# Performance work log

Hardware: AMD Instinct MI355X
Metric: run time of the kernel (lower is better)

## Reference

```python
import jax, jax.numpy as jnp
import numpy as np

EMBED_DIM = 256
NUM_HEADS = 4
HEAD_DIM = EMBED_DIM // NUM_HEADS
B, N0, N1 = 4, 2048, 2048


def setup_inputs() -> dict:
    key = jax.random.key(0)
    ks = jax.random.split(key, 16)
    d = EMBED_DIM
    s = 0.02
    return {
        "x0": jax.random.normal(ks[0], (B, N0, d), jnp.float32),
        "x1": jax.random.normal(ks[1], (B, N1, d), jnp.float32),
        "Wqk": jax.random.normal(ks[2], (d, d), jnp.float32) * s,
        "bqk": jnp.zeros((d,), jnp.float32),
        "Wv": jax.random.normal(ks[3], (d, d), jnp.float32) * s,
        "bv": jnp.zeros((d,), jnp.float32),
        "Wout": jax.random.normal(ks[4], (d, d), jnp.float32) * s,
        "bout": jnp.zeros((d,), jnp.float32),
        "W0": jax.random.normal(ks[5], (2 * d, 2 * d), jnp.float32) * s,
        "b0": jnp.zeros((2 * d,), jnp.float32),
        "ln_scale": jnp.ones((2 * d,), jnp.float32),
        "ln_bias": jnp.zeros((2 * d,), jnp.float32),
        "W3": jax.random.normal(ks[6], (2 * d, d), jnp.float32) * s,
        "b3": jnp.zeros((d,), jnp.float32),
    }


def _heads(t, b, n):
    # [b, n, d] -> [b, h, n, hd]
    return t.reshape(b, n, NUM_HEADS, HEAD_DIM).transpose(0, 2, 1, 3)


def _layernorm(y, scale, bias, eps=1e-5):
    mu = jnp.mean(y, axis=-1, keepdims=True)
    var = jnp.mean(jnp.square(y - mu), axis=-1, keepdims=True)
    return (y - mu) * jax.lax.rsqrt(var + eps) * scale + bias


def reference(x0, x1, Wqk, bqk, Wv, bv, Wout, bout, W0, b0, ln_scale, ln_bias, W3, b3):
    b, n0, d = x0.shape
    _, n1, _ = x1.shape
    scale = 1.0 / jnp.sqrt(jnp.float32(HEAD_DIM))

    qk0 = _heads(x0 @ Wqk + bqk, b, n0)
    qk1 = _heads(x1 @ Wqk + bqk, b, n1)
    v0 = _heads(x0 @ Wv + bv, b, n0)
    v1 = _heads(x1 @ Wv + bv, b, n1)

    # shared logits: [b, h, n0, n1]
    logits01 = jnp.einsum('bhid,bhjd->bhij', qk0, qk1) * scale
    attn01 = jax.nn.softmax(logits01, axis=-1)
    m0 = jnp.einsum('bhij,bhjd->bhid', attn01, v1)
    attn10 = jax.nn.softmax(logits01.transpose(0, 1, 3, 2), axis=-1)
    m1 = jnp.einsum('bhji,bhjd->bhid', attn10.transpose(0, 1, 3, 2), v0)

    m0 = m0.transpose(0, 2, 1, 3).reshape(b, n0, d) @ Wout + bout
    m1 = m1.transpose(0, 2, 1, 3).reshape(b, n1, d) @ Wout + bout

    def ffn(x, m):
        y = jnp.concatenate([x, m], axis=-1) @ W0 + b0
        y = _layernorm(y, ln_scale, ln_bias)
        y = jax.nn.gelu(y, approximate=False)
        return x + y @ W3 + b3

    return ffn(x0, m0), ffn(x1, m1)
```

## Files before the change

### kernel.cpp

```cpp
#include <hip/hip_runtime.h>
#include <math.h>

#define BATCH 4
#define SEQ 2048
#define DMODEL 256
#define NH 4
#define HD 64
#define MROWS 8192
#define QKSCALE 0.4246608905f

typedef short bf16x8 __attribute__((ext_vector_type(8)));
typedef float f32x4 __attribute__((ext_vector_type(4)));
typedef unsigned short us;

#if __has_builtin(__builtin_amdgcn_exp2f)
#define EXP2(x) __builtin_amdgcn_exp2f(x)
#else
#define EXP2(x) exp2f(x)
#endif

__device__ __forceinline__ us f2bf(float x) {
  union { float f; unsigned int u; } v;
  v.f = x;
  unsigned int r = (v.u + 0x7FFF + ((v.u >> 16) & 1)) >> 16;
  return (us)r;
}
__device__ __forceinline__ float bf2f(us u) {
  union { unsigned int u; float f; } v;
  v.u = ((unsigned int)u) << 16;
  return v.f;
}
__device__ __forceinline__ unsigned int fbits(float x) {
  union { float f; unsigned int u; } v;
  v.f = x;
  return v.u;
}
__device__ __forceinline__ unsigned int pk2bf(float lo, float hi) {
  return __builtin_amdgcn_perm(fbits(hi), fbits(lo), 0x07060302u);
}
__device__ __forceinline__ void dma16(const void* g, void* l) {
  auto gp = (const __attribute__((address_space(1))) unsigned int*)(unsigned long long)(uintptr_t)g;
  auto lp = (__attribute__((address_space(3))) unsigned int*)(unsigned int)(uintptr_t)l;
  __builtin_amdgcn_global_load_lds(gp, lp, 16, 0, 0);
}

__global__ __launch_bounds__(256) void prep_k(
    const float* __restrict__ x0, const float* __restrict__ x1,
    const float* __restrict__ Wqk, const float* __restrict__ Wv,
    const float* __restrict__ W0, const float* __restrict__ W3,
    const float* __restrict__ Wout,
    const float* __restrict__ bqk, const float* __restrict__ bv,
    const float* __restrict__ b0, const float* __restrict__ bout,
    us* __restrict__ x0b, us* __restrict__ x1b,
    us* __restrict__ Wqvt, us* __restrict__ W1t, us* __restrict__ W3t,
    float* __restrict__ bias_qv, float* __restrict__ bias1) {
  const int bid = blockIdx.x, t = threadIdx.x;
  if (bid < 4096) {
    const int n4 = (MROWS * DMODEL) / 4;
    int i = bid * 256 + t;
    const float* src = (i < n4) ? x0 : x1;
    us* dst = (i < n4) ? x0b : x1b;
    int j = (i < n4) ? i : i - n4;
    float4 v = *(const float4*)&src[j * 4];
    ushort4 o = {f2bf(v.x), f2bf(v.y), f2bf(v.z), f2bf(v.w)};
    *(ushort4*)&dst[j * 4] = o;
  } else if (bid < 5634) {
    int gid = (bid - 4096) * 256 + t;
    if (gid < 65536) {
      int k = gid >> 8, j = gid & 255;
      Wqvt[j * 256 + k] = f2bf(Wqk[gid]);
    } else if (gid < 131072) {
      int i = gid - 65536;
      int k = i >> 8, j = i & 255;
      Wqvt[(256 + j) * 256 + k] = f2bf(Wv[i]);
    } else if (gid < 262144) {
      int i = gid - 131072;
      int k = i >> 9, j = i & 511;
      W1t[j * 512 + k] = f2bf(W0[i]);
    } else if (gid < 393216) {
      int i = gid - 262144;
      int k = i >> 8, j = i & 255;
      W3t[j * 512 + k] = f2bf(W3[i]);
    } else if (gid < 393728) {
      int j = gid - 393216;
      bias_qv[j] = (j < 256) ? bqk[j] : bv[j - 256];
    }
  } else {
    int i = bid - 5634;
    if (i < 256) {
      float a0 = 0.f, a1 = 0.f;
      for (int k0 = 0; k0 < 256; k0 += 8) {
        float wk[8], r0[8], r1[8];
#pragma unroll
        for (int u = 0; u < 8; ++u) {
          wk[u] = Wout[i * 256 + k0 + u];
          const float* row = &W0[(size_t)(256 + k0 + u) * 512];
          r0[u] = row[t];
          r1[u] = row[t + 256];
        }
#pragma unroll
        for (int u = 0; u < 8; ++u) { a0 += wk[u] * r0[u]; a1 += wk[u] * r1[u]; }
      }
      W1t[t * 512 + 256 + i] = f2bf(a0);
      W1t[(t + 256) * 512 + 256 + i] = f2bf(a1);
    } else {
      float a0 = b0[t], a1 = b0[t + 256];
      for (int k = 0; k < 256; ++k) {
        float bk = bout[k];
        const float* row = &W0[(size_t)(256 + k) * 512];
        a0 += bk * row[t];
        a1 += bk * row[t + 256];
      }
      bias1[t] = a0;
      bias1[t + 256] = a1;
    }
  }
}

template <int MODE>
__global__ __launch_bounds__(256) void gemm5(
    const us* __restrict__ A0, const us* __restrict__ A1,
    const us* __restrict__ Am0, const us* __restrict__ Am1,
    const us* __restrict__ Wt, const float* __restrict__ bias,
    const float* __restrict__ r0_, const float* __restrict__ r1_,
    void* __restrict__ C0_, void* __restrict__ C1_,
    void* __restrict__ V0_, void* __restrict__ V1_, int K) {
  constexpr int CT = (MODE == 2) ? 64 : 128;
  constexpr int BG = (CT / 16) * 2;
  constexpr int BUFS = 8192 + BG * 512;
  __shared__ us lds[2 * BUFS];

  const int t = threadIdx.x, w = t >> 6, lane = t & 63;
  const int qd = lane >> 4, l15 = lane & 15;

  const int flat = blockIdx.x + 64 * (blockIdx.y + 4 * blockIdx.z);
  const int xcd = flat & 7, slot = flat >> 3;
  const int xz = (xcd << 4) + (slot >> 2);
  const int bx = xz & 63, z = xz >> 6, coltile = slot & 3;
  const int row0 = bx * 128, col0 = coltile * CT;

  const us* Ax = z ? A1 : A0;
  const us* Am = z ? Am1 : Am0;
  const int qr = (MODE == 2) ? w : (w >> 1);
  const int qc = (MODE == 2) ? 0 : (w & 1);
  constexpr int MI = (MODE == 2) ? 2 : 4;

  f32x4 acc[MI][4];
#pragma unroll
  for (int i = 0; i < MI; ++i)
#pragma unroll
    for (int j = 0; j < 4; ++j) acc[i][j] = (f32x4){0.f, 0.f, 0.f, 0.f};

  const int NK = K >> 6;
#pragma unroll
  for (int pp = 0; pp < (16 + BG) / 4; ++pp) {
    int g = pp * 4 + w;
    const us* src;
    if (g < 16) {
      int tm = g >> 1, s = g & 1;
      int kk = s * 32 + qd * 8;
      src = &((MODE == 1) ? Ax : Ax)[(size_t)(row0 + tm * 16 + l15) * ((MODE == 1) ? 256 : K) + kk];
    } else {
      int gb = g - 16, tn = gb >> 1, s = gb & 1;
      src = &Wt[(size_t)(col0 + tn * 16 + l15) * K + s * 32 + qd * 8];
    }
    dma16(src, &lds[g * 512]);
  }
  __syncthreads();

  int bsel = 0;
  for (int it = 0; it < NK; ++it) {
    if (it + 1 < NK) {
      int k0 = (it + 1) << 6;
#pragma unroll
      for (int pp = 0; pp < (16 + BG) / 4; ++pp) {
        int g = pp * 4 + w;
        const us* src;
        if (g < 16) {
          int tm = g >> 1, s = g & 1;
          const us* Ap = Ax;
          int kk = k0 + s * 32 + qd * 8, lda = K;
          if (MODE == 1) {
            Ap = (k0 < 256) ? Ax : Am;
            kk &= 255;
            lda = 256;
          }
          src = &Ap[(size_t)(row0 + tm * 16 + l15) * lda + kk];
        } else {
          int gb = g - 16, tn = gb >> 1, s = gb & 1;
          src = &Wt[(size_t)(col0 + tn * 16 + l15) * K + k0 + s * 32 + qd * 8];
        }
        dma16(src, &lds[(bsel ^ 1) * BUFS + g * 512]);
      }
    }
    const us* L = &lds[bsel * BUFS];
#pragma unroll
    for (int s = 0; s < 2; ++s) {
      bf16x8 af[MI], bfr[4];
#pragma unroll
      for (int i = 0; i < MI; ++i)
        af[i] = *(const bf16x8*)&L[(((qr * MI + i) * 2 + s) * 64 + lane) * 8];
#pragma unroll
      for (int j = 0; j < 4; ++j)
        bfr[j] = *(const bf16x8*)&L[8192 + (((qc * 4 + j) * 2 + s) * 64 + lane) * 8];
#pragma unroll
      for (int i = 0; i < MI; ++i)
#pragma unroll
        for (int j = 0; j < 4; ++j)
          acc[i][j] = __builtin_amdgcn_mfma_f32_16x16x32_bf16(af[i], bfr[j], acc[i][j], 0, 0, 0);
    }
    __syncthreads();
    bsel ^= 1;
  }

  if (MODE == 0 && coltile >= 2) {
    int base = qc * 8320;
#pragma unroll
    for (int j = 0; j < 4; ++j) {
      int col = col0 + qc * 64 + j * 16 + l15;
      float bb = bias[col];
#pragma unroll
      for (int i = 0; i < 4; ++i)
#pragma unroll
        for (int r = 0; r < 4; ++r)
          lds[base + (j * 16 + l15) * 130 + (qr * 64 + i * 16 + qd * 4 + r)] =
              f2bf(acc[i][j][r] + bb);
    }
    __syncthreads();
    us* Vt = (us*)(z ? V1_ : V0_);
    int b_ = row0 >> 11, seq0 = row0 & 2047;
    for (int c = t; c < 2048; c += 256) {
      int hh = c >> 10, cc = c & 1023;
      int dloc = cc >> 4, scc = cc & 15;
      int h = (coltile - 2) * 2 + hh;
      uint4 d = *(const uint4*)&lds[hh * 8320 + dloc * 130 + scc * 8];
      *(uint4*)&Vt[((size_t)(b_ * NH + h) * HD + dloc) * SEQ + seq0 + scc * 8] = d;
    }
    return;
  }

#pragma unroll
  for (int j = 0; j < 4; ++j) {
    int col = col0 + qc * 64 + j * 16 + l15;
    float bb = bias[col];
#pragma unroll
    for (int i = 0; i < MI; ++i)
#pragma unroll
      for (int r = 0; r < 4; ++r) {
        size_t grow = row0 + qr * (MI * 16) + i * 16 + qd * 4 + r;
        float v = acc[i][j][r] + bb;
        if (MODE == 0) {
          ((us*)(z ? C1_ : C0_))[grow * 256 + col] = f2bf(v * QKSCALE);
        } else if (MODE == 1) {
          ((us*)(z ? C1_ : C0_))[grow * 512 + col] = f2bf(v);
        } else {
          const float* R = z ? r1_ : r0_;
          ((float*)(z ? C1_ : C0_))[grow * 256 + col] = R[grow * 256 + col] + v;
        }
      }
  }
}

__global__ __launch_bounds__(256) void flash_v7(
    const us* __restrict__ qk0, const us* __restrict__ qk1,
    const us* __restrict__ vt0, const us* __restrict__ vt1,
    float* __restrict__ Opart, float* __restrict__ lpart) {
  __shared__ us lds[16384];
  const int t = threadIdx.x, w = t >> 6, lane = t & 63;
  const int qd = lane >> 4, l15 = lane & 15;

  const int flat = blockIdx.x + 32 * (blockIdx.y + 4 * blockIdx.z);
  const int xcd = flat & 7, slot = flat >> 3;
  const int combo = (xcd << 2) + (slot >> 5);
  const int qs = slot & 31;
  const int qt = qs & 15, half = qs >> 4;
  const int dir = combo >> 4, bh = combo & 15, b = bh >> 2, h = bh & 3;

  const us* Qb = dir ? qk1 : qk0;
  const us* Kb = dir ? qk0 : qk1;
  const us* Vt = dir ? vt0 : vt1;
  float* Op = Opart + (size_t)(dir * 2 + half) * (MROWS * DMODEL);
  float* lp = lpart + ((size_t)(dir * 2 + half) * NH + h) * MROWS;
  const size_t qrow0 = (size_t)b * SEQ + (size_t)qt * 128;
  const int hoff = h * HD;
  const us* vtb = Vt + (size_t)(b * NH + h) * HD * SEQ;
  const int kt0 = half * 16;

  const us* sp[4];
  int sstr[4];
#pragma unroll
  for (int pp = 0; pp < 4; ++pp) {
    int g = pp * 4 + w;
    if (g < 8) {
      int tk = g >> 1, s = g & 1;
      int kvl = (tk >> 1) * 32 + (l15 >> 2) * 8 + (tk & 1) * 4 + (l15 & 3);
      sp[pp] = &Kb[(size_t)(b * SEQ + kt0 * 64 + kvl) * DMODEL + hoff + s * 32 + qd * 8];
      sstr[pp] = 64 * DMODEL;
    } else {
      int td = (g - 8) >> 1, s = g & 1;
      sp[pp] = &vtb[(size_t)(td * 16 + l15) * SEQ + kt0 * 64 + s * 32 + qd * 8];
      sstr[pp] = 64;
    }
  }

  bf16x8 qf[2][2];
#pragma unroll
  for (int qh = 0; qh < 2; ++qh)
#pragma unroll
    for (int s = 0; s < 2; ++s)
      qf[qh][s] = *(const bf16x8*)&Qb[(qrow0 + w * 32 + qh * 16 + l15) * DMODEL + hoff + s * 32 + qd * 8];

  f32x4 Oacc[2][4];
#pragma unroll
  for (int qh = 0; qh < 2; ++qh)
#pragma unroll
    for (int td = 0; td < 4; ++td) Oacc[qh][td] = (f32x4){0.f, 0.f, 0.f, 0.f};
  float l_lane[2] = {0.f, 0.f};

#pragma unroll
  for (int pp = 0; pp < 4; ++pp) {
    dma16(sp[pp], &lds[(pp * 4 + w) * 512]);
    sp[pp] += sstr[pp];
  }
  __syncthreads();

  int bsel = 0;
  for (int it = 0; it < 16; ++it) {
    if (it < 15) {
#pragma unroll
      for (int pp = 0; pp < 4; ++pp) {
        dma16(sp[pp], &lds[(bsel ^ 1) * 8192 + (pp * 4 + w) * 512]);
        sp[pp] += sstr[pp];
      }
    }
    const us* L = &lds[bsel * 8192];

    bf16x8 kf[4][2], vf[4][2];
#pragma unroll
    for (int tk = 0; tk < 4; ++tk)
#pragma unroll
      for (int s = 0; s < 2; ++s) {
        kf[tk][s] = *(const bf16x8*)&L[((tk * 2 + s) * 64 + lane) * 8];
        vf[tk][s] = *(const bf16x8*)&L[((8 + tk * 2 + s) * 64 + lane) * 8];
      }

#pragma unroll
    for (int qh = 0; qh < 2; ++qh) {
      f32x4 S[4];
#pragma unroll
      for (int tk = 0; tk < 4; ++tk) {
        f32x4 a = {0.f, 0.f, 0.f, 0.f};
        a = __builtin_amdgcn_mfma_f32_16x16x32_bf16(kf[tk][0], qf[qh][0], a, 0, 0, 0);
        a = __builtin_amdgcn_mfma_f32_16x16x32_bf16(kf[tk][1], qf[qh][1], a, 0, 0, 0);
        S[tk] = a;
      }
      float p[4][4];
      float rs = 0.f;
#pragma unroll
      for (int tk = 0; tk < 4; ++tk)
#pragma unroll
        for (int r = 0; r < 4; ++r) {
          float pv = EXP2(S[tk][r]);
          p[tk][r] = pv;
          rs += pv;
        }
      l_lane[qh] += rs;
      union { bf16x8 v; unsigned int u[4]; } pk0, pk1;
      pk0.u[0] = pk2bf(p[0][0], p[0][1]);
      pk0.u[1] = pk2bf(p[0][2], p[0][3]);
      pk0.u[2] = pk2bf(p[1][0], p[1][1]);
      pk0.u[3] = pk2bf(p[1][2], p[1][3]);
      pk1.u[0] = pk2bf(p[2][0], p[2][1]);
      pk1.u[1] = pk2bf(p[2][2], p[2][3]);
      pk1.u[2] = pk2bf(p[3][0], p[3][1]);
      pk1.u[3] = pk2bf(p[3][2], p[3][3]);
#pragma unroll
      for (int td = 0; td < 4; ++td) {
        Oacc[qh][td] = __builtin_amdgcn_mfma_f32_16x16x32_bf16(pk0.v, vf[td][0], Oacc[qh][td], 0, 0, 0);
        Oacc[qh][td] = __builtin_amdgcn_mfma_f32_16x16x32_bf16(pk1.v, vf[td][1], Oacc[qh][td], 0, 0, 0);
      }
    }
    __syncthreads();
    bsel ^= 1;
  }

#pragma unroll
  for (int qh = 0; qh < 2; ++qh) {
    float l = l_lane[qh];
    l += __shfl_xor(l, 16);
    l += __shfl_xor(l, 32);
    if (qd == 0) lp[qrow0 + w * 32 + qh * 16 + l15] = l;
#pragma unroll
    for (int r = 0; r < 4; ++r) {
      size_t row = qrow0 + w * 32 + qh * 16 + qd * 4 + r;
#pragma unroll
      for (int td = 0; td < 4; ++td)
        Op[row * DMODEL + hoff + td * 16 + l15] = Oacc[qh][td][r];
    }
  }
}

__global__ __launch_bounds__(256) void combine_k(
    const float* __restrict__ Opart, const float* __restrict__ lpart,
    us* __restrict__ m0b, us* __restrict__ m1b) {
  int gid = blockIdx.x * 256 + threadIdx.x;
  int dir = gid >= (MROWS * DMODEL / 4);
  int idx = gid - dir * (MROWS * DMODEL / 4);
  int row = idx >> 6;
  int c4 = (idx & 63) << 2;
  int h = c4 >> 6;
  const float* Oa = Opart + (size_t)(dir * 2 + 0) * (MROWS * DMODEL);
  const float* Ob = Opart + (size_t)(dir * 2 + 1) * (MROWS * DMODEL);
  float la = lpart[((size_t)(dir * 2 + 0) * NH + h) * MROWS + row];
  float lb = lpart[((size_t)(dir * 2 + 1) * NH + h) * MROWS + row];
  float inv = 1.0f / (la + lb);
  float4 a = *(const float4*)&Oa[(size_t)row * DMODEL + c4];
  float4 bv = *(const float4*)&Ob[(size_t)row * DMODEL + c4];
  us* m = dir ? m1b : m0b;
  ushort4 o = {f2bf((a.x + bv.x) * inv), f2bf((a.y + bv.y) * inv),
               f2bf((a.z + bv.z) * inv), f2bf((a.w + bv.w) * inv)};
  *(ushort4*)&m[(size_t)row * DMODEL + c4] = o;
}

__global__ __launch_bounds__(256) void ln_gelu3(
    us* __restrict__ Y0, us* __restrict__ Y1,
    const float* __restrict__ sc, const float* __restrict__ bi) {
  int w = threadIdx.x >> 6, lane = threadIdx.x & 63;
  int ridx = blockIdx.x * 4 + w;
  us* Y = (ridx >= MROWS) ? Y1 : Y0;
  int row = ridx & (MROWS - 1);
  us* p = Y + (size_t)row * 512 + lane * 8;
  uint4 u = *(const uint4*)p;
  unsigned int uu[4] = {u.x, u.y, u.z, u.w};
  float v[8];
#pragma unroll
  for (int i = 0; i < 4; ++i) {
    v[2 * i] = bf2f((us)(uu[i] & 0xFFFF));
    v[2 * i + 1] = bf2f((us)(uu[i] >> 16));
  }
  float s1 = 0.f, s2 = 0.f;
#pragma unroll
  for (int i = 0; i < 8; ++i) { s1 += v[i]; s2 += v[i] * v[i]; }
#pragma unroll
  for (int m = 1; m < 64; m <<= 1) {
    s1 += __shfl_xor(s1, m);
    s2 += __shfl_xor(s2, m);
  }
  float mu = s1 * (1.0f / 512.0f);
  float var = s2 * (1.0f / 512.0f) - mu * mu;
  float rstd = rsqrtf(var + 1e-5f);
  int c0 = lane * 8;
  float4 scA = *(const float4*)&sc[c0], scB = *(const float4*)&sc[c0 + 4];
  float4 biA = *(const float4*)&bi[c0], biB = *(const float4*)&bi[c0 + 4];
  float scv[8] = {scA.x, scA.y, scA.z, scA.w, scB.x, scB.y, scB.z, scB.w};
  float biv[8] = {biA.x, biA.y, biA.z, biA.w, biB.x, biB.y, biB.z, biB.w};
  unsigned int ou[4];
#pragma unroll
  for (int i = 0; i < 4; ++i) {
    float y0 = (v[2 * i] - mu) * rstd * scv[2 * i] + biv[2 * i];
    float y1 = (v[2 * i + 1] - mu) * rstd * scv[2 * i + 1] + biv[2 * i + 1];
    y0 = 0.5f * y0 * (1.0f + erff(y0 * 0.70710678118654752f));
    y1 = 0.5f * y1 * (1.0f + erff(y1 * 0.70710678118654752f));
    ou[i] = (unsigned int)f2bf(y0) | ((unsigned int)f2bf(y1) << 16);
  }
  uint4 o = {ou[0], ou[1], ou[2], ou[3]};
  *(uint4*)p = o;
}

extern "C" void kernel_launch(void* const* d_in, const int* in_sizes, int n_in,
                              void* d_out, int out_size, void* d_ws,
                              size_t ws_size, hipStream_t stream) {
  const float* x0   = (const float*)d_in[0];
  const float* x1   = (const float*)d_in[1];
  const float* Wqk  = (const float*)d_in[2];
  const float* bqk  = (const float*)d_in[3];
  const float* Wv   = (const float*)d_in[4];
  const float* bv   = (const float*)d_in[5];
  const float* Wout = (const float*)d_in[6];
  const float* bout = (const float*)d_in[7];
  const float* W0   = (const float*)d_in[8];
  const float* b0   = (const float*)d_in[9];
  const float* lns  = (const float*)d_in[10];
  const float* lnb  = (const float*)d_in[11];
  const float* W3   = (const float*)d_in[12];
  const float* b3   = (const float*)d_in[13];

  char* ws = (char*)d_ws;
  const size_t MB = 1024 * 1024;
  us* x0b  = (us*)(ws + 0 * MB);
  us* x1b  = (us*)(ws + 4 * MB);
  us* Wqvt = (us*)(ws + 8 * MB);
  us* W1t  = (us*)(ws + 8 * MB + 262144);
  us* W3t  = (us*)(ws + 8 * MB + 786432);
  float* bias_qv = (float*)(ws + 9 * MB);
  float* bias1   = (float*)(ws + 9 * MB + 4096);
  us* qk0b = (us*)(ws + 10 * MB);
  us* qk1b = (us*)(ws + 14 * MB);
  us* vt0  = (us*)(ws + 18 * MB);
  us* vt1  = (us*)(ws + 22 * MB);
  us* m0b  = (us*)(ws + 26 * MB);
  us* m1b  = (us*)(ws + 30 * MB);
  us* y0b  = (us*)(ws + 10 * MB);
  us* y1b  = (us*)(ws + 18 * MB);
  float* Opart = (float*)(ws + 34 * MB);
  float* lpart = (float*)(ws + 66 * MB);
  float* out0 = (float*)d_out;
  float* out1 = out0 + (size_t)MROWS * DMODEL;

  dim3 blk(256);

  prep_k<<<dim3(5891), blk, 0, stream>>>(x0, x1, Wqk, Wv, W0, W3, Wout,
                                         bqk, bv, b0, bout,
                                         x0b, x1b, Wqvt, W1t, W3t,
                                         bias_qv, bias1);

  gemm5<0><<<dim3(64, 4, 2), blk, 0, stream>>>(
      x0b, x1b, nullptr, nullptr, Wqvt, bias_qv, nullptr, nullptr,
      qk0b, qk1b, vt0, vt1, 256);

  flash_v7<<<dim3(32, 4, 8), blk, 0, stream>>>(qk0b, qk1b, vt0, vt1, Opart, lpart);
  combine_k<<<dim3(4096), blk, 0, stream>>>(Opart, lpart, m0b, m1b);

  gemm5<1><<<dim3(64, 4, 2), blk, 0, stream>>>(
      x0b, x1b, m0b, m1b, W1t, bias1, nullptr, nullptr,
      y0b, y1b, nullptr, nullptr, 512);

  ln_gelu3<<<dim3(4096), blk, 0, stream>>>(y0b, y1b, lns, lnb);

  gemm5<2><<<dim3(64, 4, 2), blk, 0, stream>>>(
      y0b, y1b, nullptr, nullptr, W3t, b3, x0, x1,
      out0, out1, nullptr, nullptr, 512);
}
```

Baseline: 233.3 us.

## Replace double-buffered DMA GEMM with single-buffer 128x64 tile GEMM

The GEMM kernel is rewritten to use a fixed 128x64 output tile for all modes, loading through registers into a single LDS buffer instead of double-buffered direct-to-LDS async copies. The XCD-aware block swizzle is dropped in favour of plain grid indexing, and the QK/V and FFN1 GEMMs launch twice as many column tiles. This lowers LDS use and may raise occupancy, but it gives up load/compute overlap and the L2 locality from the swizzle.

```diff
diff --git a/kernel.cpp b/kernel.cpp
--- a/kernel.cpp
+++ b/kernel.cpp
@@ -118,137 +118,110 @@
 }
 
 template <int MODE>
-__global__ __launch_bounds__(256) void gemm5(
-    const us* __restrict__ A0, const us* __restrict__ A1,
-    const us* __restrict__ Am0, const us* __restrict__ Am1,
+__global__ __launch_bounds__(256) void gemm8(
+    const us* __restrict__ A_0, const us* __restrict__ A_1,
+    const us* __restrict__ A2_0, const us* __restrict__ A2_1,
     const us* __restrict__ Wt, const float* __restrict__ bias,
     const float* __restrict__ r0_, const float* __restrict__ r1_,
     void* __restrict__ C0_, void* __restrict__ C1_,
     void* __restrict__ V0_, void* __restrict__ V1_, int K) {
-  constexpr int CT = (MODE == 2) ? 64 : 128;
-  constexpr int BG = (CT / 16) * 2;
-  constexpr int BUFS = 8192 + BG * 512;
-  __shared__ us lds[2 * BUFS];
-
-  const int t = threadIdx.x, w = t >> 6, lane = t & 63;
+  __shared__ us lds[12288];
+
+  const int t = threadIdx.x;
+  const int w = t >> 6, lane = t & 63;
   const int qd = lane >> 4, l15 = lane & 15;
-
-  const int flat = blockIdx.x + 64 * (blockIdx.y + 4 * blockIdx.z);
-  const int xcd = flat & 7, slot = flat >> 3;
-  const int xz = (xcd << 4) + (slot >> 2);
-  const int bx = xz & 63, z = xz >> 6, coltile = slot & 3;
-  const int row0 = bx * 128, col0 = coltile * CT;
-
-  const us* Ax = z ? A1 : A0;
-  const us* Am = z ? Am1 : Am0;
-  const int qr = (MODE == 2) ? w : (w >> 1);
-  const int qc = (MODE == 2) ? 0 : (w & 1);
-  constexpr int MI = (MODE == 2) ? 2 : 4;
-
-  f32x4 acc[MI][4];
-#pragma unroll
-  for (int i = 0; i < MI; ++i)
-#pragma unroll
-    for (int j = 0; j < 4; ++j) acc[i][j] = (f32x4){0.f, 0.f, 0.f, 0.f};
-
-  const int NK = K >> 6;
-#pragma unroll
-  for (int pp = 0; pp < (16 + BG) / 4; ++pp) {
-    int g = pp * 4 + w;
-    const us* src;
-    if (g < 16) {
-      int tm = g >> 1, s = g & 1;
-      int kk = s * 32 + qd * 8;
-      src = &((MODE == 1) ? Ax : Ax)[(size_t)(row0 + tm * 16 + l15) * ((MODE == 1) ? 256 : K) + kk];
-    } else {
-      int gb = g - 16, tn = gb >> 1, s = gb & 1;
-      src = &Wt[(size_t)(col0 + tn * 16 + l15) * K + s * 32 + qd * 8];
-    }
-    dma16(src, &lds[g * 512]);
-  }
-  __syncthreads();
-
-  int bsel = 0;
-  for (int it = 0; it < NK; ++it) {
-    if (it + 1 < NK) {
-      int k0 = (it + 1) << 6;
-#pragma unroll
-      for (int pp = 0; pp < (16 + BG) / 4; ++pp) {
-        int g = pp * 4 + w;
-        const us* src;
-        if (g < 16) {
-          int tm = g >> 1, s = g & 1;
-          const us* Ap = Ax;
-          int kk = k0 + s * 32 + qd * 8, lda = K;
-          if (MODE == 1) {
-            Ap = (k0 < 256) ? Ax : Am;
-            kk &= 255;
-            lda = 256;
-          }
-          src = &Ap[(size_t)(row0 + tm * 16 + l15) * lda + kk];
-        } else {
-          int gb = g - 16, tn = gb >> 1, s = gb & 1;
-          src = &Wt[(size_t)(col0 + tn * 16 + l15) * K + k0 + s * 32 + qd * 8];
+  const int row0 = blockIdx.x * 128;
+  const int coltile = blockIdx.y, col0 = coltile * 64;
+  const int z = blockIdx.z;
+  const us* A = z ? A_1 : A_0;
+  const us* A2 = z ? A2_1 : A2_0;
+
+  f32x4 acc[2][4];
+#pragma unroll
+  for (int mh = 0; mh < 2; ++mh)
+#pragma unroll
+    for (int tn = 0; tn < 4; ++tn) acc[mh][tn] = (f32x4){0.f, 0.f, 0.f, 0.f};
+
+  for (int k0 = 0; k0 < K; k0 += 64) {
+    __syncthreads();
+#pragma unroll
+    for (int pp = 0; pp < 6; ++pp) {
+      int g = pp * 4 + w;
+      uint4 d;
+      if (g < 16) {
+        int tm = g >> 1, s = g & 1;
+        const us* Ap = A;
+        int kk = k0 + s * 32 + qd * 8, lda = K;
+        if (MODE == 1) {
+          Ap = (k0 < 256) ? A : A2;
+          kk = (k0 & 255) + s * 32 + qd * 8;
+          lda = 256;
         }
-        dma16(src, &lds[(bsel ^ 1) * BUFS + g * 512]);
-      }
-    }
-    const us* L = &lds[bsel * BUFS];
-#pragma unroll
-    for (int s = 0; s < 2; ++s) {
-      bf16x8 af[MI], bfr[4];
-#pragma unroll
-      for (int i = 0; i < MI; ++i)
-        af[i] = *(const bf16x8*)&L[(((qr * MI + i) * 2 + s) * 64 + lane) * 8];
-#pragma unroll
-      for (int j = 0; j < 4; ++j)
-        bfr[j] = *(const bf16x8*)&L[8192 + (((qc * 4 + j) * 2 + s) * 64 + lane) * 8];
-#pragma unroll
-      for (int i = 0; i < MI; ++i)
-#pragma unroll
-        for (int j = 0; j < 4; ++j)
-          acc[i][j] = __builtin_amdgcn_mfma_f32_16x16x32_bf16(af[i], bfr[j], acc[i][j], 0, 0, 0);
+        d = *(const uint4*)&Ap[(size_t)(row0 + tm * 16 + l15) * lda + kk];
+        *(uint4*)&lds[(g * 64 + lane) * 8] = d;
+      } else {
+        int tn = (g - 16) >> 1, s = g & 1;
+        d = *(const uint4*)&Wt[(size_t)(col0 + tn * 16 + l15) * K + k0 + s * 32 + qd * 8];
+        *(uint4*)&lds[8192 + (((tn * 2 + s) * 64 + lane)) * 8] = d;
+      }
     }
     __syncthreads();
-    bsel ^= 1;
-  }
-
-  if (MODE == 0 && coltile >= 2) {
-    int base = qc * 8320;
-#pragma unroll
-    for (int j = 0; j < 4; ++j) {
-      int col = col0 + qc * 64 + j * 16 + l15;
+
+    bf16x8 aA[2][2];
+#pragma unroll
+    for (int mh = 0; mh < 2; ++mh)
+#pragma unroll
+      for (int s = 0; s < 2; ++s)
+        aA[mh][s] = *(const bf16x8*)&lds[((((w * 2 + mh) * 2 + s)) * 64 + lane) * 8];
+#pragma unroll
+    for (int tn = 0; tn < 4; ++tn) {
+      bf16x8 b0v = *(const bf16x8*)&lds[8192 + ((tn * 2 + 0) * 64 + lane) * 8];
+      bf16x8 b1v = *(const bf16x8*)&lds[8192 + ((tn * 2 + 1) * 64 + lane) * 8];
+#pragma unroll
+      for (int mh = 0; mh < 2; ++mh) {
+        acc[mh][tn] = __builtin_amdgcn_mfma_f32_16x16x32_bf16(aA[mh][0], b0v, acc[mh][tn], 0, 0, 0);
+        acc[mh][tn] = __builtin_amdgcn_mfma_f32_16x16x32_bf16(aA[mh][1], b1v, acc[mh][tn], 0, 0, 0);
+      }
+    }
+  }
+
+  if (MODE == 0 && coltile >= 4) {
+    __syncthreads();
+    int h_ = coltile - 4;
+#pragma unroll
+    for (int tn = 0; tn < 4; ++tn) {
+      int col = col0 + tn * 16 + l15;
       float bb = bias[col];
 #pragma unroll
-      for (int i = 0; i < 4; ++i)
-#pragma unroll
-        for (int r = 0; r < 4; ++r)
-          lds[base + (j * 16 + l15) * 130 + (qr * 64 + i * 16 + qd * 4 + r)] =
-              f2bf(acc[i][j][r] + bb);
+      for (int mh = 0; mh < 2; ++mh)
+#pragma unroll
+        for (int r = 0; r < 4; ++r) {
+          int rloc = w * 32 + mh * 16 + qd * 4 + r;
+          lds[(tn * 16 + l15) * 130 + rloc] = f2bf(acc[mh][tn][r] + bb);
+        }
     }
     __syncthreads();
     us* Vt = (us*)(z ? V1_ : V0_);
-    int b_ = row0 >> 11, seq0 = row0 & 2047;
-    for (int c = t; c < 2048; c += 256) {
-      int hh = c >> 10, cc = c & 1023;
-      int dloc = cc >> 4, scc = cc & 15;
-      int h = (coltile - 2) * 2 + hh;
-      uint4 d = *(const uint4*)&lds[hh * 8320 + dloc * 130 + scc * 8];
-      *(uint4*)&Vt[((size_t)(b_ * NH + h) * HD + dloc) * SEQ + seq0 + scc * 8] = d;
+    int b_ = row0 >> 11;
+    int seq0 = row0 & 2047;
+    for (int c = t; c < 1024; c += 256) {
+      int dloc = c >> 4, scc = c & 15;
+      uint4 d = *(const uint4*)&lds[dloc * 130 + scc * 8];
+      *(uint4*)&Vt[((size_t)(b_ * NH + h_) * HD + dloc) * SEQ + seq0 + scc * 8] = d;
     }
     return;
   }
 
 #pragma unroll
-  for (int j = 0; j < 4; ++j) {
-    int col = col0 + qc * 64 + j * 16 + l15;
+  for (int tn = 0; tn < 4; ++tn) {
+    int col = col0 + tn * 16 + l15;
     float bb = bias[col];
 #pragma unroll
-    for (int i = 0; i < MI; ++i)
+    for (int mh = 0; mh < 2; ++mh)
 #pragma unroll
       for (int r = 0; r < 4; ++r) {
-        size_t grow = row0 + qr * (MI * 16) + i * 16 + qd * 4 + r;
-        float v = acc[i][j][r] + bb;
+        size_t grow = row0 + w * 32 + mh * 16 + qd * 4 + r;
+        float v = acc[mh][tn][r] + bb;
         if (MODE == 0) {
           ((us*)(z ? C1_ : C0_))[grow * 256 + col] = f2bf(v * QKSCALE);
         } else if (MODE == 1) {
@@ -514,20 +487,20 @@
                                          x0b, x1b, Wqvt, W1t, W3t,
                                          bias_qv, bias1);
 
-  gemm5<0><<<dim3(64, 4, 2), blk, 0, stream>>>(
+  gemm8<0><<<dim3(64, 8, 2), blk, 0, stream>>>(
       x0b, x1b, nullptr, nullptr, Wqvt, bias_qv, nullptr, nullptr,
       qk0b, qk1b, vt0, vt1, 256);
 
   flash_v7<<<dim3(32, 4, 8), blk, 0, stream>>>(qk0b, qk1b, vt0, vt1, Opart, lpart);
   combine_k<<<dim3(4096), blk, 0, stream>>>(Opart, lpart, m0b, m1b);
 
-  gemm5<1><<<dim3(64, 4, 2), blk, 0, stream>>>(
+  gemm8<1><<<dim3(64, 8, 2), blk, 0, stream>>>(
       x0b, x1b, m0b, m1b, W1t, bias1, nullptr, nullptr,
       y0b, y1b, nullptr, nullptr, 512);
 
   ln_gelu3<<<dim3(4096), blk, 0, stream>>>(y0b, y1b, lns, lnb);
 
-  gemm5<2><<<dim3(64, 4, 2), blk, 0, stream>>>(
+  gemm8<2><<<dim3(64, 4, 2), blk, 0, stream>>>(
       y0b, y1b, nullptr, nullptr, W3t, b3, x0, x1,
       out0, out1, nullptr, nullptr, 512);
 }
```

New measurement: 243.3 us. 4.3% more time.
